# Performance work log

Hardware: AMD Instinct MI355X
Metric: run time of the kernel (lower is better)

Reference implementation:

```python
import itertools
import jax, jax.numpy as jnp
import numpy as np

# ---- JPEG constants (match utils.y_table / utils.c_table) ----
_Y_TABLE = np.array([
    [16, 11, 10, 16, 24, 40, 51, 61],
    [12, 12, 14, 19, 26, 58, 60, 55],
    [14, 13, 16, 24, 40, 57, 69, 56],
    [14, 17, 22, 29, 51, 87, 80, 62],
    [18, 22, 37, 56, 68, 109, 103, 77],
    [24, 35, 55, 64, 81, 104, 113, 92],
    [49, 64, 78, 87, 103, 121, 120, 101],
    [72, 92, 95, 98, 112, 100, 103, 99]], dtype=np.float32)
_C_TABLE = np.full((8, 8), 99, dtype=np.float32)
_C_TABLE[:4, :4] = np.array([[17, 18, 24, 47], [18, 21, 26, 66],
                             [24, 26, 56, 99], [47, 66, 99, 99]], dtype=np.float32)

# RGB -> YCbCr matrix (code defines M then uses M.T via tensordot dims=1)
_YCBCR_M = np.array([[0.299, 0.587, 0.114],
                     [-0.168736, -0.331264, 0.5],
                     [0.5, -0.418688, -0.081312]], dtype=np.float32)
_SHIFT = np.array([0.0, 128.0, 128.0], dtype=np.float32)

_cx = np.cos((2 * np.arange(8)[:, None] + 1) * np.arange(8)[None, :] * np.pi / 16)  # [x,u]
_DCT = np.einsum('xu,yv->xyuv', _cx, _cx).astype(np.float32)
_alpha = np.array([1.0 / np.sqrt(2)] + [1.0] * 7)
_DCT_SCALE = (np.outer(_alpha, _alpha) * 0.25).astype(np.float32)

FACTOR = 1.0
K = 8  # block size


def _block_split(x):
    # x: [B, H, W] -> [B, H*W/64, 8, 8]
    B, H, W = x.shape
    x = x.reshape(B, H // K, K, W // K, K)
    x = jnp.transpose(x, (0, 1, 3, 2, 4))
    return x.reshape(B, -1, K, K)


def _dct_8x8(x):
    # x: [B, N, 8, 8]
    x = x - 128.0
    return jnp.asarray(_DCT_SCALE) * jnp.einsum('bnxy,xyuv->bnuv', x, jnp.asarray(_DCT))


def _avg_pool2(x):
    # 2x2 average pooling, stride 2; x: [B, H, W]
    B, H, W = x.shape
    return x.reshape(B, H // 2, 2, W // 2, 2).mean(axis=(2, 4))


def _compress(image):
    # image: [B, 3, H, W] in [0, 1]
    img = jnp.transpose(image * 255.0, (0, 2, 3, 1))  # [B, H, W, 3]
    ycbcr = jnp.einsum('bhwc,cd->bhwd', img, jnp.asarray(_YCBCR_M.T)) + jnp.asarray(_SHIFT)
    y = ycbcr[..., 0]
    cb = _avg_pool2(ycbcr[..., 1])
    cr = _avg_pool2(ycbcr[..., 2])
    y_q = jnp.round(_dct_8x8(_block_split(y)) / (jnp.asarray(_Y_TABLE) * FACTOR))
    cb_q = jnp.round(_dct_8x8(_block_split(cb)) / (jnp.asarray(_C_TABLE) * FACTOR))
    cr_q = jnp.round(_dct_8x8(_block_split(cr)) / (jnp.asarray(_C_TABLE) * FACTOR))
    return y_q, cb_q, cr_q


def setup_inputs() -> dict:
    key = jax.random.key(0)
    image = jax.random.uniform(key, (32, 3, 512, 512), dtype=jnp.float32)
    return {"image": image}


def reference(image):
    return _compress(image)
```

## Files before the change

kernel.cpp:

```cpp
#include <hip/hip_runtime.h>
#include <cmath>


namespace jc {

constexpr double c1 = 0.98078528040323044912618223613424;
constexpr double c2 = 0.92387953251128675612818318939679;
constexpr double c3 = 0.83146961230254523707878837761791;
constexpr double c4 = 0.70710678118654752440084436210485;
constexpr double c5 = 0.55557023301960222474283081394853;
constexpr double c6 = 0.38268343236508977172845998403040;
constexpr double c7 = 0.19509032201612826784828486847702;
constexpr double alpha0 = 0.70710678118654746171979706919384;

struct Tab {
  float tr[4096];
  float sc[64];
  float yq[64];
  float cq[64];
  constexpr Tab() : tr(), sc(), yq(), cq() {
    const double CX[8][8] = {
      {1.0,  c1,  c2,  c3,  c4,  c5,  c6,  c7},
      {1.0,  c3,  c6, -c7, -c4, -c1, -c2, -c5},
      {1.0,  c5, -c6, -c1, -c4,  c7,  c2,  c3},
      {1.0,  c7, -c2, -c5,  c4,  c3, -c6, -c1},
      {1.0, -c7, -c2,  c5,  c4, -c3, -c6,  c1},
      {1.0, -c5, -c6,  c1, -c4, -c7,  c2, -c3},
      {1.0, -c3,  c6,  c7, -c4,  c1, -c2,  c5},
      {1.0, -c1,  c2, -c3,  c4, -c5,  c6, -c7}};
    for (int i = 0; i < 64; ++i) {
      const int u = i >> 3, v = i & 7;
      for (int j = 0; j < 64; ++j) {
        const int x = j >> 3, y = j & 7;
        tr[i * 64 + j] = (float)(CX[x][u] * CX[y][v]);
      }
      const double au = (u == 0) ? alpha0 : 1.0;
      const double av = (v == 0) ? alpha0 : 1.0;
      sc[i] = (float)((au * av) * 0.25);
    }
    const int YT[64] = {
      16, 11, 10, 16, 24, 40, 51, 61,
      12, 12, 14, 19, 26, 58, 60, 55,
      14, 13, 16, 24, 40, 57, 69, 56,
      14, 17, 22, 29, 51, 87, 80, 62,
      18, 22, 37, 56, 68, 109, 103, 77,
      24, 35, 55, 64, 81, 104, 113, 92,
      49, 64, 78, 87, 103, 121, 120, 101,
      72, 92, 95, 98, 112, 100, 103, 99};
    const int CT[64] = {
      17, 18, 24, 47, 99, 99, 99, 99,
      18, 21, 26, 66, 99, 99, 99, 99,
      24, 26, 56, 99, 99, 99, 99, 99,
      47, 66, 99, 99, 99, 99, 99, 99,
      99, 99, 99, 99, 99, 99, 99, 99,
      99, 99, 99, 99, 99, 99, 99, 99,
      99, 99, 99, 99, 99, 99, 99, 99,
      99, 99, 99, 99, 99, 99, 99, 99};
    for (int i = 0; i < 64; ++i) {
      yq[i] = (float)YT[i];
      cq[i] = (float)CT[i];
    }
  }
};

}

__constant__ jc::Tab TT;

__device__ __forceinline__ float vmul(float a, float b) {
  float r; asm("v_mul_f32 %0, %1, %2" : "=v"(r) : "v"(a), "v"(b)); return r;
}
__device__ __forceinline__ float vadd(float a, float b) {
  float r; asm("v_add_f32 %0, %1, %2" : "=v"(r) : "v"(a), "v"(b)); return r;
}
__device__ __forceinline__ float vsubf(float a, float b) {
  float r; asm("v_sub_f32 %0, %1, %2" : "=v"(r) : "v"(a), "v"(b)); return r;
}

__device__ __forceinline__ float chro_t(float tR, float tG, float tB,
                                        float kR, float kG, float kB) {
  float a = vmul(tR, kR);
  a = vadd(a, vmul(tG, kG));
  a = vadd(a, vmul(tB, kB));
  return vadd(a, 128.0f);
}

__device__ __forceinline__ float q4(float acc, float sc, float q) {
  return rintf(__fdiv_rn(vmul(sc, acc), q));
}


#define MP(AK, SJ, VJ) \
  "v_mul_f32 v104, " SJ ", " VJ "\n\t" \
  "v_add_f32 " AK ", " AK ", v104\n\t"

#define CHAIN(AK) \
  "v_mul_f32 " AK ", s36, v40\n\t" \
  MP(AK,"s37","v41") MP(AK,"s38","v42") MP(AK,"s39","v43") MP(AK,"s40","v44") \
  MP(AK,"s41","v45") MP(AK,"s42","v46") MP(AK,"s43","v47") \
  MP(AK,"s44","v48") MP(AK,"s45","v49") MP(AK,"s46","v50") MP(AK,"s47","v51") \
  MP(AK,"s48","v52") MP(AK,"s49","v53") MP(AK,"s50","v54") MP(AK,"s51","v55") \
  MP(AK,"s52","v56") MP(AK,"s53","v57") MP(AK,"s54","v58") MP(AK,"s55","v59") \
  MP(AK,"s56","v60") MP(AK,"s57","v61") MP(AK,"s58","v62") MP(AK,"s59","v63") \
  MP(AK,"s60","v64") MP(AK,"s61","v65") MP(AK,"s62","v66") MP(AK,"s63","v67") \
  MP(AK,"s64","v68") MP(AK,"s65","v69") MP(AK,"s66","v70") MP(AK,"s67","v71") \
  MP(AK,"s68","v72") MP(AK,"s69","v73") MP(AK,"s70","v74") MP(AK,"s71","v75") \
  MP(AK,"s72","v76") MP(AK,"s73","v77") MP(AK,"s74","v78") MP(AK,"s75","v79") \
  MP(AK,"s76","v80") MP(AK,"s77","v81") MP(AK,"s78","v82") MP(AK,"s79","v83") \
  MP(AK,"s80","v84") MP(AK,"s81","v85") MP(AK,"s82","v86") MP(AK,"s83","v87") \
  MP(AK,"s84","v88") MP(AK,"s85","v89") MP(AK,"s86","v90") MP(AK,"s87","v91") \
  MP(AK,"s88","v92") MP(AK,"s89","v93") MP(AK,"s90","v94") MP(AK,"s91","v95") \
  MP(AK,"s92","v96") MP(AK,"s93","v97") MP(AK,"s94","v98") MP(AK,"s95","v99") \
  MP(AK,"s96","v100") MP(AK,"s97","v101") MP(AK,"s98","v102") MP(AK,"s99","v103")

#define ROWM(AK, O0, O1, O2, O3) \
  "s_load_dwordx16 s[36:51], %[tp], " O0 "\n\t" \
  "s_load_dwordx16 s[52:67], %[tp], " O1 "\n\t" \
  "s_load_dwordx16 s[68:83], %[tp], " O2 "\n\t" \
  "s_load_dwordx16 s[84:99], %[tp], " O3 "\n\t" \
  "s_waitcnt lgkmcnt(0)\n\t" \
  CHAIN(AK)

#define XLOAD \
  "ds_read_b128 v[40:43], %[xa] offset:0\n\t" \
  "ds_read_b128 v[44:47], %[xa] offset:16\n\t" \
  "ds_read_b128 v[48:51], %[xa] offset:32\n\t" \
  "ds_read_b128 v[52:55], %[xa] offset:48\n\t" \
  "ds_read_b128 v[56:59], %[xa] offset:64\n\t" \
  "ds_read_b128 v[60:63], %[xa] offset:80\n\t" \
  "ds_read_b128 v[64:67], %[xa] offset:96\n\t" \
  "ds_read_b128 v[68:71], %[xa] offset:112\n\t" \
  "ds_read_b128 v[72:75], %[xa] offset:128\n\t" \
  "ds_read_b128 v[76:79], %[xa] offset:144\n\t" \
  "ds_read_b128 v[80:83], %[xa] offset:160\n\t" \
  "ds_read_b128 v[84:87], %[xa] offset:176\n\t" \
  "ds_read_b128 v[88:91], %[xa] offset:192\n\t" \
  "ds_read_b128 v[92:95], %[xa] offset:208\n\t" \
  "ds_read_b128 v[96:99], %[xa] offset:224\n\t" \
  "ds_read_b128 v[100:103], %[xa] offset:240\n\t"

#define VCLOB \
  "v40","v41","v42","v43","v44","v45","v46","v47","v48","v49", \
  "v50","v51","v52","v53","v54","v55","v56","v57","v58","v59", \
  "v60","v61","v62","v63","v64","v65","v66","v67","v68","v69", \
  "v70","v71","v72","v73","v74","v75","v76","v77","v78","v79", \
  "v80","v81","v82","v83","v84","v85","v86","v87","v88","v89", \
  "v90","v91","v92","v93","v94","v95","v96","v97","v98","v99", \
  "v100","v101","v102","v103","v104"

#define SCLOB \
  "s36","s37","s38","s39","s40","s41","s42","s43","s44","s45", \
  "s46","s47","s48","s49","s50","s51","s52","s53","s54","s55", \
  "s56","s57","s58","s59","s60","s61","s62","s63","s64","s65", \
  "s66","s67","s68","s69","s70","s71","s72","s73","s74","s75", \
  "s76","s77","s78","s79","s80","s81","s82","s83","s84","s85", \
  "s86","s87","s88","s89","s90","s91","s92","s93","s94","s95", \
  "s96","s97","s98","s99"

#define DCT16(AA, TPX) \
  asm volatile( \
    XLOAD \
    ROWM("%[a0]",  "0","64","128","192") \
    ROWM("%[a1]",  "256","320","384","448") \
    ROWM("%[a2]",  "512","576","640","704") \
    ROWM("%[a3]",  "768","832","896","960") \
    ROWM("%[a4]",  "1024","1088","1152","1216") \
    ROWM("%[a5]",  "1280","1344","1408","1472") \
    ROWM("%[a6]",  "1536","1600","1664","1728") \
    ROWM("%[a7]",  "1792","1856","1920","1984") \
    ROWM("%[a8]",  "2048","2112","2176","2240") \
    ROWM("%[a9]",  "2304","2368","2432","2496") \
    ROWM("%[a10]", "2560","2624","2688","2752") \
    ROWM("%[a11]", "2816","2880","2944","3008") \
    ROWM("%[a12]", "3072","3136","3200","3264") \
    ROWM("%[a13]", "3328","3392","3456","3520") \
    ROWM("%[a14]", "3584","3648","3712","3776") \
    ROWM("%[a15]", "3840","3904","3968","4032") \
    : [a0]"=&v"(AA##0),  [a1]"=&v"(AA##1),  [a2]"=&v"(AA##2),  [a3]"=&v"(AA##3), \
      [a4]"=&v"(AA##4),  [a5]"=&v"(AA##5),  [a6]"=&v"(AA##6),  [a7]"=&v"(AA##7), \
      [a8]"=&v"(AA##8),  [a9]"=&v"(AA##9),  [a10]"=&v"(AA##10),[a11]"=&v"(AA##11), \
      [a12]"=&v"(AA##12),[a13]"=&v"(AA##13),[a14]"=&v"(AA##14),[a15]"=&v"(AA##15) \
    : [xa]"v"(xaddr), [tp]"s"(TPX) \
    : "memory", VCLOB, SCLOB)

__global__ __launch_bounds__(256, 4)
void jpeg_kernel(const float* __restrict__ img, float* __restrict__ out) {
  __shared__ float LDSbuf[96 * 68];

  const int t = threadIdx.x;
  const int lane = t & 63;
  const int w = __builtin_amdgcn_readfirstlane(t >> 6);
  const int wid = blockIdx.x;
  const int b = wid >> 6;
  const int r = wid & 63;

  {
    const int yb = t & 63;
    const int q = t >> 6;
    const int by = yb >> 3, bx = yb & 7;
    const int prow = (r >> 3) * 64 + by * 8 + 2 * q;
    const int pcol = (r & 7) * 64 + bx * 8;
    const float* rp = img + (size_t)b * 786432 + (size_t)prow * 512 + pcol;

    float tv[3][2][8];
#pragma unroll
    for (int c = 0; c < 3; ++c) {
#pragma unroll
      for (int rr = 0; rr < 2; ++rr) {
        const float* p0 = rp + c * 262144 + rr * 512;
        const float4 va = *(const float4*)(p0);
        const float4 vb = *(const float4*)(p0 + 4);
        tv[c][rr][0] = vmul(va.x, 255.0f);
        tv[c][rr][1] = vmul(va.y, 255.0f);
        tv[c][rr][2] = vmul(va.z, 255.0f);
        tv[c][rr][3] = vmul(va.w, 255.0f);
        tv[c][rr][4] = vmul(vb.x, 255.0f);
        tv[c][rr][5] = vmul(vb.y, 255.0f);
        tv[c][rr][6] = vmul(vb.z, 255.0f);
        tv[c][rr][7] = vmul(vb.w, 255.0f);
      }
    }
#pragma unroll
    for (int rr = 0; rr < 2; ++rr) {
#pragma unroll
      for (int y = 0; y < 8; ++y) {
        float a = vmul(tv[0][rr][y], 0.299f);
        a = vadd(a, vmul(tv[1][rr][y], 0.587f));
        a = vadd(a, vmul(tv[2][rr][y], 0.114f));
        LDSbuf[yb * 68 + 16 * q + rr * 8 + y] = vsubf(a, 128.0f);
      }
    }
    const int lcr = 4 * by + q;
#pragma unroll
    for (int pc = 0; pc < 4; ++pc) {
      const int lcc = 4 * bx + pc;
      const int crow = 64 + ((lcr >> 3) * 4 + (lcc >> 3));
      const int cell = (lcr & 7) * 8 + (lcc & 7);
      const int e = 2 * pc, o = 2 * pc + 1;
      {
        const float p00 = chro_t(tv[0][0][e], tv[1][0][e], tv[2][0][e], -0.168736f, -0.331264f, 0.5f);
        const float p01 = chro_t(tv[0][0][o], tv[1][0][o], tv[2][0][o], -0.168736f, -0.331264f, 0.5f);
        const float p10 = chro_t(tv[0][1][e], tv[1][1][e], tv[2][1][e], -0.168736f, -0.331264f, 0.5f);
        const float p11 = chro_t(tv[0][1][o], tv[1][1][o], tv[2][1][o], -0.168736f, -0.331264f, 0.5f);
        const float s = vadd(vadd(vadd(p00, p01), p10), p11);
        LDSbuf[crow * 68 + cell] = vsubf(vmul(s, 0.25f), 128.0f);
      }
      {
        const float p00 = chro_t(tv[0][0][e], tv[1][0][e], tv[2][0][e], 0.5f, -0.418688f, -0.081312f);
        const float p01 = chro_t(tv[0][0][o], tv[1][0][o], tv[2][0][o], 0.5f, -0.418688f, -0.081312f);
        const float p10 = chro_t(tv[0][1][e], tv[1][1][e], tv[2][1][e], 0.5f, -0.418688f, -0.081312f);
        const float p11 = chro_t(tv[0][1][o], tv[1][1][o], tv[2][1][o], 0.5f, -0.418688f, -0.081312f);
        const float s = vadd(vadd(vadd(p00, p01), p10), p11);
        LDSbuf[(crow + 16) * 68 + cell] = vsubf(vmul(s, 0.25f), 128.0f);
      }
    }
  }

  const int ibase = (w & 1) * 32;
  const bool chro = (w >= 2);
  const bool active = (!chro) || (lane < 32);
  const int blk = chro ? (64 + (lane & 31)) : lane;
  const float* qt = chro ? TT.cq : TT.yq;

  const unsigned xaddr = (unsigned)(size_t)(&LDSbuf[blk * 68]);
  const float* tp0 = TT.tr + (size_t)(ibase) * 64;
  const float* tp1 = TT.tr + (size_t)(ibase + 16) * 64;

  float aa0, aa1, aa2, aa3, aa4, aa5, aa6, aa7;
  float aa8, aa9, aa10, aa11, aa12, aa13, aa14, aa15;
  float bb0, bb1, bb2, bb3, bb4, bb5, bb6, bb7;
  float bb8, bb9, bb10, bb11, bb12, bb13, bb14, bb15;

  __syncthreads();

  if (active) {
    DCT16(aa, tp0);
    DCT16(bb, tp1);
  }

  __syncthreads();

  const int ybase = b * 4096 + (r >> 3) * 512 + (r & 7) * 8;
  const int cbase = b * 1024 + (r >> 3) * 128 + (r & 7) * 4;

#define QSTORE(A, B, C, D, G, CO) do { \
    float4 v4_; \
    v4_.x = q4(A, TT.sc[(CO) + 4*(G) + 0], qt[(CO) + 4*(G) + 0]); \
    v4_.y = q4(B, TT.sc[(CO) + 4*(G) + 1], qt[(CO) + 4*(G) + 1]); \
    v4_.z = q4(C, TT.sc[(CO) + 4*(G) + 2], qt[(CO) + 4*(G) + 2]); \
    v4_.w = q4(D, TT.sc[(CO) + 4*(G) + 3], qt[(CO) + 4*(G) + 3]); \
    *(float4*)&LDSbuf[(w * 64 + lane) * 20 + 4*(G)] = v4_; \
  } while (0)

  {
    const int co = ibase;
    if (active) {
      QSTORE(aa0,  aa1,  aa2,  aa3,  0, co);
      QSTORE(aa4,  aa5,  aa6,  aa7,  1, co);
      QSTORE(aa8,  aa9,  aa10, aa11, 2, co);
      QSTORE(aa12, aa13, aa14, aa15, 3, co);
    }
    if (!chro) {
#pragma unroll
      for (int k = 0; k < 4; ++k) {
        const int B = k * 16 + (lane >> 2);
        const int e0 = (lane & 3) * 4;
        const float4 vv = *(const float4*)&LDSbuf[(w * 64 + B) * 20 + e0];
        const unsigned ob = (unsigned)(ybase + (B >> 3) * 64 + (B & 7));
        *(float4*)&out[(ob << 6) + (unsigned)(co + e0)] = vv;
      }
    } else {
#pragma unroll
      for (int k = 0; k < 2; ++k) {
        const int idx = k * 64 + lane;
        const int B = idx >> 2;
        const int e0 = (idx & 3) * 4;
        const float4 vv = *(const float4*)&LDSbuf[(w * 64 + B) * 20 + e0];
        const int cc = B & 15;
        const unsigned ob = 8388608u + (B >= 16 ? 2097152u : 0u) +
            (((unsigned)(cbase + (cc >> 2) * 32 + (cc & 3))) << 6);
        *(float4*)&out[ob + (unsigned)(co + e0)] = vv;
      }
    }
  }

  {
    const int co = ibase + 16;
    if (active) {
      QSTORE(bb0,  bb1,  bb2,  bb3,  0, co);
      QSTORE(bb4,  bb5,  bb6,  bb7,  1, co);
      QSTORE(bb8,  bb9,  bb10, bb11, 2, co);
      QSTORE(bb12, bb13, bb14, bb15, 3, co);
    }
    if (!chro) {
#pragma unroll
      for (int k = 0; k < 4; ++k) {
        const int B = k * 16 + (lane >> 2);
        const int e0 = (lane & 3) * 4;
        const float4 vv = *(const float4*)&LDSbuf[(w * 64 + B) * 20 + e0];
        const unsigned ob = (unsigned)(ybase + (B >> 3) * 64 + (B & 7));
        *(float4*)&out[(ob << 6) + (unsigned)(co + e0)] = vv;
      }
    } else {
#pragma unroll
      for (int k = 0; k < 2; ++k) {
        const int idx = k * 64 + lane;
        const int B = idx >> 2;
        const int e0 = (idx & 3) * 4;
        const float4 vv = *(const float4*)&LDSbuf[(w * 64 + B) * 20 + e0];
        const int cc = B & 15;
        const unsigned ob = 8388608u + (B >= 16 ? 2097152u : 0u) +
            (((unsigned)(cbase + (cc >> 2) * 32 + (cc & 3))) << 6);
        *(float4*)&out[ob + (unsigned)(co + e0)] = vv;
      }
    }
  }
#undef QSTORE
}

extern "C" void kernel_launch(void* const* d_in, const int* in_sizes, int n_in,
                              void* d_out, int out_size, void* d_ws, size_t ws_size,
                              hipStream_t stream) {
  (void)in_sizes; (void)n_in; (void)d_ws; (void)ws_size; (void)out_size;
  const float* img = (const float*)d_in[0];
  float* out = (float*)d_out;
  jpeg_kernel<<<dim3(2048), dim3(256), 0, stream>>>(img, out);
}
```

Measured before the change: 192.8 us.

## Double-buffer scalar coefficient loads and interleave two DCT output chains

Reworks the inline-asm DCT matmul so that scalar coefficient loads for the next quarter are issued before computing with the current quarter, splitting SGPRs into two halves used alternately. This overlaps s_load latency with VALU work, where the old code stalled on lgkmcnt(0) before each output row. It also computes two output accumulators at once, giving independent mul/add chains that hide VALU dependency latency. The final prefetch reads past the 4096-float table (offsets 4096/4352 land in sc/yq), which is harmless but wasted, and one extra VGPR is used.

```diff
diff --git a/kernel.cpp b/kernel.cpp
--- a/kernel.cpp
+++ b/kernel.cpp
@@ -90,36 +90,71 @@
 }
 
 
-#define MP(AK, SJ, VJ) \
-  "v_mul_f32 v104, " SJ ", " VJ "\n\t" \
-  "v_add_f32 " AK ", " AK ", v104\n\t"
-
-#define CHAIN(AK) \
-  "v_mul_f32 " AK ", s36, v40\n\t" \
-  MP(AK,"s37","v41") MP(AK,"s38","v42") MP(AK,"s39","v43") MP(AK,"s40","v44") \
-  MP(AK,"s41","v45") MP(AK,"s42","v46") MP(AK,"s43","v47") \
-  MP(AK,"s44","v48") MP(AK,"s45","v49") MP(AK,"s46","v50") MP(AK,"s47","v51") \
-  MP(AK,"s48","v52") MP(AK,"s49","v53") MP(AK,"s50","v54") MP(AK,"s51","v55") \
-  MP(AK,"s52","v56") MP(AK,"s53","v57") MP(AK,"s54","v58") MP(AK,"s55","v59") \
-  MP(AK,"s56","v60") MP(AK,"s57","v61") MP(AK,"s58","v62") MP(AK,"s59","v63") \
-  MP(AK,"s60","v64") MP(AK,"s61","v65") MP(AK,"s62","v66") MP(AK,"s63","v67") \
-  MP(AK,"s64","v68") MP(AK,"s65","v69") MP(AK,"s66","v70") MP(AK,"s67","v71") \
-  MP(AK,"s68","v72") MP(AK,"s69","v73") MP(AK,"s70","v74") MP(AK,"s71","v75") \
-  MP(AK,"s72","v76") MP(AK,"s73","v77") MP(AK,"s74","v78") MP(AK,"s75","v79") \
-  MP(AK,"s76","v80") MP(AK,"s77","v81") MP(AK,"s78","v82") MP(AK,"s79","v83") \
-  MP(AK,"s80","v84") MP(AK,"s81","v85") MP(AK,"s82","v86") MP(AK,"s83","v87") \
-  MP(AK,"s84","v88") MP(AK,"s85","v89") MP(AK,"s86","v90") MP(AK,"s87","v91") \
-  MP(AK,"s88","v92") MP(AK,"s89","v93") MP(AK,"s90","v94") MP(AK,"s91","v95") \
-  MP(AK,"s92","v96") MP(AK,"s93","v97") MP(AK,"s94","v98") MP(AK,"s95","v99") \
-  MP(AK,"s96","v100") MP(AK,"s97","v101") MP(AK,"s98","v102") MP(AK,"s99","v103")
-
-#define ROWM(AK, O0, O1, O2, O3) \
-  "s_load_dwordx16 s[36:51], %[tp], " O0 "\n\t" \
-  "s_load_dwordx16 s[52:67], %[tp], " O1 "\n\t" \
-  "s_load_dwordx16 s[68:83], %[tp], " O2 "\n\t" \
-  "s_load_dwordx16 s[84:99], %[tp], " O3 "\n\t" \
+#define MAC4(AA, AB, SA, SB, XJ) \
+  "v_mul_f32 v104, " SA ", " XJ "\n\t" \
+  "v_mul_f32 v105, " SB ", " XJ "\n\t" \
+  "v_add_f32 " AA ", " AA ", v104\n\t" \
+  "v_add_f32 " AB ", " AB ", v105\n\t"
+
+#define CH0I(AA, AB) \
+  "v_mul_f32 " AA ", s36, v40\n\t" \
+  "v_mul_f32 " AB ", s52, v40\n\t" \
+  MAC4(AA,AB,"s37","s53","v41") MAC4(AA,AB,"s38","s54","v42") \
+  MAC4(AA,AB,"s39","s55","v43") MAC4(AA,AB,"s40","s56","v44") \
+  MAC4(AA,AB,"s41","s57","v45") MAC4(AA,AB,"s42","s58","v46") \
+  MAC4(AA,AB,"s43","s59","v47") MAC4(AA,AB,"s44","s60","v48") \
+  MAC4(AA,AB,"s45","s61","v49") MAC4(AA,AB,"s46","s62","v50") \
+  MAC4(AA,AB,"s47","s63","v51") MAC4(AA,AB,"s48","s64","v52") \
+  MAC4(AA,AB,"s49","s65","v53") MAC4(AA,AB,"s50","s66","v54") \
+  MAC4(AA,AB,"s51","s67","v55")
+
+#define CH1B(AA, AB) \
+  MAC4(AA,AB,"s68","s84","v56") MAC4(AA,AB,"s69","s85","v57") \
+  MAC4(AA,AB,"s70","s86","v58") MAC4(AA,AB,"s71","s87","v59") \
+  MAC4(AA,AB,"s72","s88","v60") MAC4(AA,AB,"s73","s89","v61") \
+  MAC4(AA,AB,"s74","s90","v62") MAC4(AA,AB,"s75","s91","v63") \
+  MAC4(AA,AB,"s76","s92","v64") MAC4(AA,AB,"s77","s93","v65") \
+  MAC4(AA,AB,"s78","s94","v66") MAC4(AA,AB,"s79","s95","v67") \
+  MAC4(AA,AB,"s80","s96","v68") MAC4(AA,AB,"s81","s97","v69") \
+  MAC4(AA,AB,"s82","s98","v70") MAC4(AA,AB,"s83","s99","v71")
+
+#define CH2A(AA, AB) \
+  MAC4(AA,AB,"s36","s52","v72") MAC4(AA,AB,"s37","s53","v73") \
+  MAC4(AA,AB,"s38","s54","v74") MAC4(AA,AB,"s39","s55","v75") \
+  MAC4(AA,AB,"s40","s56","v76") MAC4(AA,AB,"s41","s57","v77") \
+  MAC4(AA,AB,"s42","s58","v78") MAC4(AA,AB,"s43","s59","v79") \
+  MAC4(AA,AB,"s44","s60","v80") MAC4(AA,AB,"s45","s61","v81") \
+  MAC4(AA,AB,"s46","s62","v82") MAC4(AA,AB,"s47","s63","v83") \
+  MAC4(AA,AB,"s48","s64","v84") MAC4(AA,AB,"s49","s65","v85") \
+  MAC4(AA,AB,"s50","s66","v86") MAC4(AA,AB,"s51","s67","v87")
+
+#define CH3B(AA, AB) \
+  MAC4(AA,AB,"s68","s84","v88") MAC4(AA,AB,"s69","s85","v89") \
+  MAC4(AA,AB,"s70","s86","v90") MAC4(AA,AB,"s71","s87","v91") \
+  MAC4(AA,AB,"s72","s88","v92") MAC4(AA,AB,"s73","s89","v93") \
+  MAC4(AA,AB,"s74","s90","v94") MAC4(AA,AB,"s75","s91","v95") \
+  MAC4(AA,AB,"s76","s92","v96") MAC4(AA,AB,"s77","s93","v97") \
+  MAC4(AA,AB,"s78","s94","v98") MAC4(AA,AB,"s79","s95","v99") \
+  MAC4(AA,AB,"s80","s96","v100") MAC4(AA,AB,"s81","s97","v101") \
+  MAC4(AA,AB,"s82","s98","v102") MAC4(AA,AB,"s83","s99","v103")
+
+#define PAIRP(AA, AB, O1A, O1B, O2A, O2B, O3A, O3B, ONA, ONB) \
   "s_waitcnt lgkmcnt(0)\n\t" \
-  CHAIN(AK)
+  "s_load_dwordx16 s[68:83], %[tp], " O1A "\n\t" \
+  "s_load_dwordx16 s[84:99], %[tp], " O1B "\n\t" \
+  CH0I(AA, AB) \
+  "s_waitcnt lgkmcnt(0)\n\t" \
+  "s_load_dwordx16 s[36:51], %[tp], " O2A "\n\t" \
+  "s_load_dwordx16 s[52:67], %[tp], " O2B "\n\t" \
+  CH1B(AA, AB) \
+  "s_waitcnt lgkmcnt(0)\n\t" \
+  "s_load_dwordx16 s[68:83], %[tp], " O3A "\n\t" \
+  "s_load_dwordx16 s[84:99], %[tp], " O3B "\n\t" \
+  CH2A(AA, AB) \
+  "s_waitcnt lgkmcnt(0)\n\t" \
+  "s_load_dwordx16 s[36:51], %[tp], " ONA "\n\t" \
+  "s_load_dwordx16 s[52:67], %[tp], " ONB "\n\t" \
+  CH3B(AA, AB)
 
 #define XLOAD \
   "ds_read_b128 v[40:43], %[xa] offset:0\n\t" \
@@ -146,7 +181,7 @@
   "v70","v71","v72","v73","v74","v75","v76","v77","v78","v79", \
   "v80","v81","v82","v83","v84","v85","v86","v87","v88","v89", \
   "v90","v91","v92","v93","v94","v95","v96","v97","v98","v99", \
-  "v100","v101","v102","v103","v104"
+  "v100","v101","v102","v103","v104","v105"
 
 #define SCLOB \
   "s36","s37","s38","s39","s40","s41","s42","s43","s44","s45", \
@@ -160,22 +195,16 @@
 #define DCT16(AA, TPX) \
   asm volatile( \
     XLOAD \
-    ROWM("%[a0]",  "0","64","128","192") \
-    ROWM("%[a1]",  "256","320","384","448") \
-    ROWM("%[a2]",  "512","576","640","704") \
-    ROWM("%[a3]",  "768","832","896","960") \
-    ROWM("%[a4]",  "1024","1088","1152","1216") \
-    ROWM("%[a5]",  "1280","1344","1408","1472") \
-    ROWM("%[a6]",  "1536","1600","1664","1728") \
-    ROWM("%[a7]",  "1792","1856","1920","1984") \
-    ROWM("%[a8]",  "2048","2112","2176","2240") \
-    ROWM("%[a9]",  "2304","2368","2432","2496") \
-    ROWM("%[a10]", "2560","2624","2688","2752") \
-    ROWM("%[a11]", "2816","2880","2944","3008") \
-    ROWM("%[a12]", "3072","3136","3200","3264") \
-    ROWM("%[a13]", "3328","3392","3456","3520") \
-    ROWM("%[a14]", "3584","3648","3712","3776") \
-    ROWM("%[a15]", "3840","3904","3968","4032") \
+    "s_load_dwordx16 s[36:51], %[tp], 0\n\t" \
+    "s_load_dwordx16 s[52:67], %[tp], 256\n\t" \
+    PAIRP("%[a0]","%[a1]",   "64","320","128","384","192","448","512","768") \
+    PAIRP("%[a2]","%[a3]",   "576","832","640","896","704","960","1024","1280") \
+    PAIRP("%[a4]","%[a5]",   "1088","1344","1152","1408","1216","1472","1536","1792") \
+    PAIRP("%[a6]","%[a7]",   "1600","1856","1664","1920","1728","1984","2048","2304") \
+    PAIRP("%[a8]","%[a9]",   "2112","2368","2176","2432","2240","2496","2560","2816") \
+    PAIRP("%[a10]","%[a11]", "2624","2880","2688","2944","2752","3008","3072","3328") \
+    PAIRP("%[a12]","%[a13]", "3136","3392","3200","3456","3264","3520","3584","3840") \
+    PAIRP("%[a14]","%[a15]", "3648","3904","3712","3968","3776","4032","4096","4352") \
     : [a0]"=&v"(AA##0),  [a1]"=&v"(AA##1),  [a2]"=&v"(AA##2),  [a3]"=&v"(AA##3), \
       [a4]"=&v"(AA##4),  [a5]"=&v"(AA##5),  [a6]"=&v"(AA##6),  [a7]"=&v"(AA##7), \
       [a8]"=&v"(AA##8),  [a9]"=&v"(AA##9),  [a10]"=&v"(AA##10),[a11]"=&v"(AA##11), \
```

New measurement: 193.5 us. No clear change (+0.4%).
